# Optimization experiments

Hardware: AMD Instinct MI355X
Metric: run time of the kernel (lower is better)

## Reference

```python
import jax, jax.numpy as jnp
import numpy as np

EPS = 1e-5  # BatchNorm1d default eps
N1, N2 = 4096, 4096


def _encoder(x, W1, b1, W2, b2, W3, b3, gamma, beta):
    # fc1: Linear(node_num,256)+ReLU; fc2: Linear(256,128)+ReLU; fc3: Linear(128,64)+BN(train-mode)+ReLU
    h = jax.nn.relu(x @ W1.T + b1)
    h = jax.nn.relu(h @ W2.T + b2)
    h = h @ W3.T + b3
    m = h.mean(axis=0)
    v = ((h - m) ** 2).mean(axis=0)  # biased variance, as BN training mode
    return jax.nn.relu((h - m) / jnp.sqrt(v + EPS) * gamma + beta)


def _self_attention(x, adj, alpha):
    # vectorized form of the per-node double loop:
    # tmp_i = (sum_{j: adj[i,j]==1} alpha[i,j] * x[j]) / degree_i + x[i]  if degree_i != 0 else 0
    mask = (adj == 1.0).astype(x.dtype)           # [N,N]
    deg = adj.sum(axis=1, keepdims=True)          # [N,1]
    agg = (mask * alpha) @ x                      # [N,64] masked SpMM
    return jnp.where(deg != 0, agg / deg + x, jnp.zeros((), x.dtype))


def setup_inputs() -> dict:
    key = jax.random.key(0)
    ks = jax.random.split(key, 20)
    d = {}
    d["x1"] = jax.random.normal(ks[0], (N1, N1), jnp.float32)
    d["x2"] = jax.random.normal(ks[1], (N2, N2), jnp.float32)
    d["adj1"] = jax.random.bernoulli(ks[2], 0.01, (N1, N1)).astype(jnp.float32)
    d["adj2"] = jax.random.bernoulli(ks[3], 0.01, (N2, N2)).astype(jnp.float32)
    def lin(k, fan_out, fan_in):
        bound = 1.0 / np.sqrt(fan_in)
        k1, k2 = jax.random.split(k)
        return (jax.random.uniform(k1, (fan_out, fan_in), jnp.float32, -bound, bound),
                jax.random.uniform(k2, (fan_out,), jnp.float32, -bound, bound))
    d["e1_W1"], d["e1_b1"] = lin(ks[4], 256, N1)
    d["e1_W2"], d["e1_b2"] = lin(ks[5], 128, 256)
    d["e1_W3"], d["e1_b3"] = lin(ks[6], 64, 128)
    d["e1_gamma"] = jnp.ones((64,), jnp.float32)
    d["e1_beta"] = jnp.zeros((64,), jnp.float32)
    d["e2_W1"], d["e2_b1"] = lin(ks[7], 256, N2)
    d["e2_W2"], d["e2_b2"] = lin(ks[8], 128, 256)
    d["e2_W3"], d["e2_b3"] = lin(ks[9], 64, 128)
    d["e2_gamma"] = jnp.ones((64,), jnp.float32)
    d["e2_beta"] = jnp.zeros((64,), jnp.float32)
    d["alpha1"] = jax.random.uniform(ks[10], (N1, N1), jnp.float32)
    d["alpha2"] = jax.random.uniform(ks[11], (N2, N2), jnp.float32)
    d["Wc"], d["bc"] = lin(ks[12], 2, (N1 + N2) * 64)
    return d


def reference(x1, x2, adj1, adj2,
              e1_W1, e1_b1, e1_W2, e1_b2, e1_W3, e1_b3, e1_gamma, e1_beta,
              e2_W1, e2_b1, e2_W2, e2_b2, e2_W3, e2_b3, e2_gamma, e2_beta,
              alpha1, alpha2, Wc, bc):
    h1 = _encoder(x1, e1_W1, e1_b1, e1_W2, e1_b2, e1_W3, e1_b3, e1_gamma, e1_beta)
    h2 = _encoder(x2, e2_W1, e2_b1, e2_W2, e2_b2, e2_W3, e2_b3, e2_gamma, e2_beta)
    h1 = _self_attention(h1, adj1, alpha1)
    h2 = _self_attention(h2, adj2, alpha2)
    feat = jnp.concatenate([h1, h2], axis=0).reshape(1, -1)  # [1,(N1+N2)*64]
    return feat @ Wc.T + bc  # [1,2] logits (softmax is defined but unused in forward)
```

## Files before the change

kernel.cpp:

```cpp
#include <hip/hip_runtime.h>
#include <cstddef>
#include <cstdint>


#define NN 4096
#define HDIM 64
#define ENC_OUT (NN * HDIM)

typedef _Float16 half8 __attribute__((ext_vector_type(8)));
typedef _Float16 half4 __attribute__((ext_vector_type(4)));
typedef float v4f __attribute__((ext_vector_type(4)));

__device__ __forceinline__ void gld_lds16(const void* g, void* l) {
    __builtin_amdgcn_global_load_lds(
        (const __attribute__((address_space(1))) void*)g,
        (__attribute__((address_space(3))) void*)l, 16, 0, 0);
}

struct GemmP {
    const void*     A[2];
    const _Float16* B[2];
    const float*    bias[2];
    void*           C[2];
};

__global__ __launch_bounds__(1024) void fc1_kernel(GemmP p)
{
    __shared__ char lds[64 * 1024];

    const int tid = threadIdx.x;
    const int wave = tid >> 6, lane = tid & 63;
    const int l16 = lane & 15, quad = lane >> 4;
    const int kg = wave >> 2, ng = wave & 3;
    const int enc = blockIdx.y;
    const int m0 = blockIdx.x * 32;
    const int kOff = kg * 1024;
    constexpr int NS = 16;

    const float* __restrict__ A = (const float*)p.A[enc];
    const _Float16* __restrict__ Bp = p.B[enc];

    const int srow = ng * 8 + (lane >> 3);
    const int sc   = lane & 7;
    const float* asrc = A + (size_t)(m0 + srow) * NN + kOff + sc * 4;

    char* f16kg = &lds[kg * 8192];
    const int wof = srow * 64 + (((sc >> 1) ^ ((srow >> 1) & 3)) * 16) + (sc & 1) * 8;

    const int r0 = l16, r1 = 16 + l16;
    const int rd0 = r0 * 64 + ((quad ^ ((r0 >> 1) & 3)) * 16);
    const int rd1 = r1 * 64 + ((quad ^ ((r1 >> 1) & 3)) * 16);

    const _Float16* bsrc = Bp + (size_t)(ng * 64 + l16) * NN + kOff + quad * 8;

    v4f acc[2][4];
#pragma unroll
    for (int mi = 0; mi < 2; mi++)
#pragma unroll
        for (int ni = 0; ni < 4; ni++) acc[mi][ni] = (v4f){0.f, 0.f, 0.f, 0.f};

    float4 aA[2], aB[2];
    aA[0] = *(const float4*)(asrc);
    aA[1] = *(const float4*)(asrc + 32);

    auto body = [&](int s, float4* cur, float4* nxt, bool last) {
        half8 b[2][4];
#pragma unroll
        for (int kq = 0; kq < 2; kq++)
#pragma unroll
            for (int ni = 0; ni < 4; ni++)
                b[kq][ni] = *(const half8*)(bsrc + (size_t)ni * 16 * NN + s * 64 + kq * 32);
        if (!last) {
            nxt[0] = *(const float4*)(asrc + (s + 1) * 64);
            nxt[1] = *(const float4*)(asrc + (s + 1) * 64 + 32);
        }
        __builtin_amdgcn_sched_barrier(0);

        char* fb = f16kg + (s & 1) * 4096;
#pragma unroll
        for (int j = 0; j < 2; j++) {
            half4 h;
            h[0] = (_Float16)cur[j].x; h[1] = (_Float16)cur[j].y;
            h[2] = (_Float16)cur[j].z; h[3] = (_Float16)cur[j].w;
            *(half4*)(fb + j * 2048 + wof) = h;
        }
        __builtin_amdgcn_s_waitcnt(0xC07F);
        __builtin_amdgcn_sched_barrier(0);
        __builtin_amdgcn_s_barrier();
        __builtin_amdgcn_sched_barrier(0);
        half8 a0k0 = *(const half8*)(fb + rd0);
        half8 a1k0 = *(const half8*)(fb + rd1);
        half8 a0k1 = *(const half8*)(fb + 2048 + rd0);
        half8 a1k1 = *(const half8*)(fb + 2048 + rd1);
#pragma unroll
        for (int ni = 0; ni < 4; ni++) {
            acc[0][ni] = __builtin_amdgcn_mfma_f32_16x16x32_f16(a0k0, b[0][ni], acc[0][ni], 0, 0, 0);
            acc[0][ni] = __builtin_amdgcn_mfma_f32_16x16x32_f16(a0k1, b[1][ni], acc[0][ni], 0, 0, 0);
            acc[1][ni] = __builtin_amdgcn_mfma_f32_16x16x32_f16(a1k0, b[0][ni], acc[1][ni], 0, 0, 0);
            acc[1][ni] = __builtin_amdgcn_mfma_f32_16x16x32_f16(a1k1, b[1][ni], acc[1][ni], 0, 0, 0);
        }
    };

    for (int s = 0; s < NS - 2; s += 2) {
        body(s, aA, aB, false);
        body(s + 1, aB, aA, false);
    }
    body(NS - 2, aA, aB, false);
    body(NS - 1, aB, aA, true);

    __syncthreads();

    if (kg >= 2) {
        const int sidx = (kg - 2) * 4 + ng;
#pragma unroll
        for (int mi = 0; mi < 2; mi++)
#pragma unroll
            for (int ni = 0; ni < 4; ni++)
                *(v4f*)&lds[sidx * 8192 + (mi * 4 + ni) * 1024 + lane * 16] = acc[mi][ni];
    }
    __syncthreads();
    if (kg < 2) {
        const int sidx = kg * 4 + ng;
#pragma unroll
        for (int mi = 0; mi < 2; mi++)
#pragma unroll
            for (int ni = 0; ni < 4; ni++)
                acc[mi][ni] += *(const v4f*)&lds[sidx * 8192 + (mi * 4 + ni) * 1024 + lane * 16];
    }
    __syncthreads();

    if (kg == 1) {
#pragma unroll
        for (int mi = 0; mi < 2; mi++)
#pragma unroll
            for (int ni = 0; ni < 4; ni++)
                *(v4f*)&lds[ng * 8192 + (mi * 4 + ni) * 1024 + lane * 16] = acc[mi][ni];
    }
    __syncthreads();

    if (kg == 0) {
        _Float16* __restrict__ h1 = (_Float16*)p.C[enc];
        const float* __restrict__ bs = p.bias[enc];
#pragma unroll
        for (int mi = 0; mi < 2; mi++)
#pragma unroll
            for (int ni = 0; ni < 4; ni++) {
                v4f v = acc[mi][ni] + *(const v4f*)&lds[ng * 8192 + (mi * 4 + ni) * 1024 + lane * 16];
                const int col = ng * 64 + ni * 16 + l16;
                const float b = bs[col];
#pragma unroll
                for (int i = 0; i < 4; i++) {
                    const int row = m0 + mi * 16 + quad * 4 + i;
                    h1[(size_t)row * 256 + col] = (_Float16)fmaxf(v[i] + b, 0.f);
                }
            }
    }
}

template<int NI, bool A16, int OUT, bool RELU>
__global__ __launch_bounds__(256) void gemm_kernel(GemmP p, int M, int lda, int Ksub)
{
    constexpr int N = NI * 64;
    __shared__ char Bs[NI * 4 * 1024];

    const int tid = threadIdx.x;
    const int wave = tid >> 6, lane = tid & 63;
    const int l16 = lane & 15, quad = lane >> 4;
    const int enc = blockIdx.z, split = blockIdx.x;
    const int m0 = blockIdx.y * 32;
    const int kOff = split * Ksub;
    const int nsteps = Ksub >> 5;

    const _Float16* __restrict__ Bp = p.B[enc];
    const char* Abase = (const char*)p.A[enc];

    const size_t aoff0 = (size_t)(m0 + l16) * lda + kOff + quad * 8;
    const size_t aoff1 = aoff0 + (size_t)16 * lda;

    half8 na0, na1;
    float4 nf0lo, nf0hi, nf1lo, nf1hi;
    auto loadA = [&](int s) {
        if constexpr (A16) {
            const _Float16* A = (const _Float16*)Abase;
            na0 = *(const half8*)(A + aoff0 + s * 32);
            na1 = *(const half8*)(A + aoff1 + s * 32);
        } else {
            const float* A = (const float*)Abase;
            nf0lo = *(const float4*)(A + aoff0 + s * 32);
            nf0hi = *(const float4*)(A + aoff0 + s * 32 + 4);
            nf1lo = *(const float4*)(A + aoff1 + s * 32);
            nf1hi = *(const float4*)(A + aoff1 + s * 32 + 4);
        }
    };

    v4f acc[2][NI];
#pragma unroll
    for (int mi = 0; mi < 2; mi++)
#pragma unroll
        for (int ni = 0; ni < NI; ni++) acc[mi][ni] = (v4f){0.f, 0.f, 0.f, 0.f};

    loadA(0);

    for (int s = 0; s < nsteps; ++s) {
#pragma unroll
        for (int ni = 0; ni < NI; ni++) {
            const int T = wave * NI + ni;
            const _Float16* g = Bp + (size_t)(T * 16 + l16) * lda + kOff + s * 32 + quad * 8;
            gld_lds16(g, &Bs[T * 1024]);
        }
        __builtin_amdgcn_sched_barrier(0);
        half8 ca0, ca1;
        if constexpr (A16) {
            ca0 = na0; ca1 = na1;
        } else {
            ca0[0] = (_Float16)nf0lo.x; ca0[1] = (_Float16)nf0lo.y;
            ca0[2] = (_Float16)nf0lo.z; ca0[3] = (_Float16)nf0lo.w;
            ca0[4] = (_Float16)nf0hi.x; ca0[5] = (_Float16)nf0hi.y;
            ca0[6] = (_Float16)nf0hi.z; ca0[7] = (_Float16)nf0hi.w;
            ca1[0] = (_Float16)nf1lo.x; ca1[1] = (_Float16)nf1lo.y;
            ca1[2] = (_Float16)nf1lo.z; ca1[3] = (_Float16)nf1lo.w;
            ca1[4] = (_Float16)nf1hi.x; ca1[5] = (_Float16)nf1hi.y;
            ca1[6] = (_Float16)nf1hi.z; ca1[7] = (_Float16)nf1hi.w;
        }
        const bool more = (s + 1 < nsteps);
        if (more) loadA(s + 1);
        __builtin_amdgcn_sched_barrier(0);

        if (more) __builtin_amdgcn_s_waitcnt(0x0F72);
        else      __builtin_amdgcn_s_waitcnt(0x0F70);
        __builtin_amdgcn_sched_barrier(0);

#pragma unroll
        for (int ni = 0; ni < NI; ni++) {
            half8 bf = *(const half8*)&Bs[(wave * NI + ni) * 1024 + lane * 16];
            acc[0][ni] = __builtin_amdgcn_mfma_f32_16x16x32_f16(ca0, bf, acc[0][ni], 0, 0, 0);
            acc[1][ni] = __builtin_amdgcn_mfma_f32_16x16x32_f16(ca1, bf, acc[1][ni], 0, 0, 0);
        }
    }

#pragma unroll
    for (int mi = 0; mi < 2; mi++)
#pragma unroll
        for (int ni = 0; ni < NI; ni++) {
            const int col = wave * NI * 16 + ni * 16 + l16;
#pragma unroll
            for (int i = 0; i < 4; i++) {
                const int row = m0 + mi * 16 + quad * 4 + i;
                float v = acc[mi][ni][i];
                v += p.bias[enc][col];
                if (RELU) v = fmaxf(v, 0.f);
                if constexpr (OUT == 0)
                    ((_Float16*)p.C[enc])[(size_t)row * N + col] = (_Float16)v;
                else
                    ((float*)p.C[enc])[(size_t)row * N + col] = v;
            }
        }
}

struct CvtJob { const float* s; _Float16* d; int n4; };
struct CvtP { CvtJob j[6]; };

__global__ __launch_bounds__(256) void cvt_all_kernel(CvtP p)
{
    int i = blockIdx.x * 256 + threadIdx.x;
#pragma unroll
    for (int k = 0; k < 6; k++) {
        if (i < p.j[k].n4) {
            float4 v = ((const float4*)p.j[k].s)[i];
            half4 h;
            h[0] = (_Float16)v.x; h[1] = (_Float16)v.y;
            h[2] = (_Float16)v.z; h[3] = (_Float16)v.w;
            ((half4*)p.j[k].d)[i] = h;
            return;
        }
        i -= p.j[k].n4;
    }
}

__global__ __launch_bounds__(256) void bn_stat1_kernel(const float* __restrict__ h3,
                                                       float* __restrict__ bnp)
{
    const int enc = blockIdx.y, b = blockIdx.x;
    const int c = threadIdx.x & 63, rg = threadIdx.x >> 6;
    const float* h = h3 + (size_t)enc * ENC_OUT + (size_t)b * 128 * HDIM;
    float s = 0.f, q = 0.f;
    for (int r = rg; r < 128; r += 4) {
        float v = h[(size_t)r * HDIM + c];
        s += v; q += v * v;
    }
    __shared__ float ss[4][64], sq[4][64];
    ss[rg][c] = s; sq[rg][c] = q;
    __syncthreads();
    if (threadIdx.x < 64) {
        float S = ss[0][c] + ss[1][c] + ss[2][c] + ss[3][c];
        float Q = sq[0][c] + sq[1][c] + sq[2][c] + sq[3][c];
        bnp[(size_t)(enc * 32 + b) * 128 + c] = S;
        bnp[(size_t)(enc * 32 + b) * 128 + 64 + c] = Q;
    }
}

__global__ void bn_stat2_kernel(const float* __restrict__ bnp, float* __restrict__ stats)
{
    const int enc = blockIdx.x, c = threadIdx.x;
    float s = 0.f, q = 0.f;
    for (int b = 0; b < 32; b++) {
        s += bnp[(size_t)(enc * 32 + b) * 128 + c];
        q += bnp[(size_t)(enc * 32 + b) * 128 + 64 + c];
    }
    float mean = s * (1.f / NN);
    float var = q * (1.f / NN) - mean * mean;
    stats[enc * 128 + c] = mean;
    stats[enc * 128 + 64 + c] = rsqrtf(var + 1e-5f);
}

__global__ __launch_bounds__(256) void bn_apply_kernel(const float* __restrict__ h3,
                                                       const float* __restrict__ stats,
                                                       const float* __restrict__ g0,
                                                       const float* __restrict__ g1,
                                                       const float* __restrict__ be0,
                                                       const float* __restrict__ be1,
                                                       float* __restrict__ hn)
{
    const int idx = blockIdx.x * 256 + threadIdx.x;
    const int enc = idx >> 18;
    const int c = idx & 63;
    const float* g = enc ? g1 : g0;
    const float* be = enc ? be1 : be0;
    const float m = stats[enc * 128 + c];
    const float rs = stats[enc * 128 + 64 + c];
    float v = (h3[idx] - m) * rs * g[c] + be[c];
    hn[idx] = fmaxf(v, 0.f);
}

__global__ __launch_bounds__(256) void att_kernel(const float* __restrict__ adj1,
                                                  const float* __restrict__ adj2,
                                                  const float* __restrict__ al1,
                                                  const float* __restrict__ al2,
                                                  const float* __restrict__ hn,
                                                  float* __restrict__ out)
{
    const int enc = blockIdx.y;
    const float* adj = enc ? adj2 : adj1;
    const float* al = enc ? al2 : al1;
    const float* h = hn + (size_t)enc * ENC_OUT;
    float* o = out + (size_t)enc * ENC_OUT;
    const int i = blockIdx.x;
    const int tid = threadIdx.x;
    const int lane = tid & 63;
    const int w = tid >> 6;

    __shared__ int s_j[192];
    __shared__ float s_w[192];
    __shared__ int s_wc[4];
    __shared__ float s_acc[4][64];

    const float* arow = adj + (size_t)i * NN;

    unsigned long long masks[16];
    int cnt_w = 0;
#pragma unroll
    for (int r = 0; r < 16; ++r) {
        float a = arow[w * 1024 + r * 64 + lane];
        unsigned long long m = __ballot(a == 1.f);
        masks[r] = m;
        cnt_w += __popcll(m);
    }
    if (lane == 0) s_wc[w] = cnt_w;
    __syncthreads();

    const int c0 = s_wc[0], c1 = s_wc[1], c2 = s_wc[2], c3 = s_wc[3];
    const int cnt = c0 + c1 + c2 + c3;
    const int cc = min(cnt, 192);
    int run = (w > 0 ? c0 : 0) + (w > 1 ? c1 : 0) + (w > 2 ? c2 : 0);

#pragma unroll
    for (int r = 0; r < 16; ++r) {
        unsigned long long m = masks[r];
        if ((m >> lane) & 1ull) {
            int pos = run + __popcll(m & ((1ull << lane) - 1ull));
            if (pos < 192) s_j[pos] = w * 1024 + r * 64 + lane;
        }
        run += __popcll(m);
    }
    __syncthreads();

    const float* alrow = al + (size_t)i * NN;
    for (int t = tid; t < cc; t += 256) s_w[t] = alrow[s_j[t]];
    __syncthreads();

    const int c = tid & 63;
    const int g = tid >> 6;
    float acc = 0.f;
    for (int t = g; t < cc; t += 4) acc += s_w[t] * h[(size_t)s_j[t] * HDIM + c];
    s_acc[g][c] = acc;
    __syncthreads();

    if (tid < 64) {
        float r;
        if (cnt != 0) {
            r = (s_acc[0][c] + s_acc[1][c] + s_acc[2][c] + s_acc[3][c]) / (float)cnt
                + h[(size_t)i * HDIM + c];
        } else {
            r = 0.f;
        }
        o[(size_t)i * HDIM + c] = r;
    }
}

#define FDIM (2 * ENC_OUT)

__global__ __launch_bounds__(256) void final_partial_kernel(const float* __restrict__ feat,
                                                            const float* __restrict__ Wc,
                                                            float* __restrict__ partial)
{
    const int gt = blockIdx.x * 256 + threadIdx.x;
    float p0 = 0.f, p1 = 0.f;
    for (int f = gt; f < FDIM; f += 131072) {
        float x = feat[f];
        p0 += x * Wc[f];
        p1 += x * Wc[FDIM + f];
    }
    __shared__ float r0[256], r1[256];
    r0[threadIdx.x] = p0;
    r1[threadIdx.x] = p1;
    __syncthreads();
    for (int off = 128; off > 0; off >>= 1) {
        if (threadIdx.x < off) {
            r0[threadIdx.x] += r0[threadIdx.x + off];
            r1[threadIdx.x] += r1[threadIdx.x + off];
        }
        __syncthreads();
    }
    if (threadIdx.x == 0) {
        partial[blockIdx.x * 2 + 0] = r0[0];
        partial[blockIdx.x * 2 + 1] = r1[0];
    }
}

__global__ __launch_bounds__(256) void final_reduce_kernel(const float* __restrict__ partial,
                                                           const float* __restrict__ bc,
                                                           float* __restrict__ out)
{
    const int t = threadIdx.x;
    float2 v = ((const float2*)partial)[t];
    float2 w = ((const float2*)partial)[t + 256];
    __shared__ float r0[256], r1[256];
    r0[t] = v.x + w.x;
    r1[t] = v.y + w.y;
    __syncthreads();
    for (int off = 128; off > 0; off >>= 1) {
        if (t < off) {
            r0[t] += r0[t + off];
            r1[t] += r1[t + off];
        }
        __syncthreads();
    }
    if (t == 0) {
        out[0] = bc[0] + r0[0];
        out[1] = bc[1] + r1[0];
    }
}


extern "C" void kernel_launch(void* const* d_in, const int* in_sizes, int n_in,
                              void* d_out, int out_size, void* d_ws, size_t ws_size,
                              hipStream_t stream)
{
    const float* x1    = (const float*)d_in[0];
    const float* x2    = (const float*)d_in[1];
    const float* adj1  = (const float*)d_in[2];
    const float* adj2  = (const float*)d_in[3];
    const float* e1_W1 = (const float*)d_in[4];
    const float* e1_b1 = (const float*)d_in[5];
    const float* e1_W2 = (const float*)d_in[6];
    const float* e1_b2 = (const float*)d_in[7];
    const float* e1_W3 = (const float*)d_in[8];
    const float* e1_b3 = (const float*)d_in[9];
    const float* e1_g  = (const float*)d_in[10];
    const float* e1_be = (const float*)d_in[11];
    const float* e2_W1 = (const float*)d_in[12];
    const float* e2_b1 = (const float*)d_in[13];
    const float* e2_W2 = (const float*)d_in[14];
    const float* e2_b2 = (const float*)d_in[15];
    const float* e2_W3 = (const float*)d_in[16];
    const float* e2_b3 = (const float*)d_in[17];
    const float* e2_g  = (const float*)d_in[18];
    const float* e2_be = (const float*)d_in[19];
    const float* alpha1 = (const float*)d_in[20];
    const float* alpha2 = (const float*)d_in[21];
    const float* Wc    = (const float*)d_in[22];
    const float* bc    = (const float*)d_in[23];
    (void)in_sizes; (void)n_in; (void)out_size; (void)ws_size;

    char* w = (char*)d_ws;
    _Float16* W1h = (_Float16*)w;  w += (size_t)2 * 256 * NN * 2;
    _Float16* W2h = (_Float16*)w;  w += (size_t)2 * 128 * 256 * 2;
    _Float16* W3h = (_Float16*)w;  w += (size_t)2 * 64 * 128 * 2;
    _Float16* h1h = (_Float16*)w;  w += (size_t)2 * NN * 256 * 2;
    char* shared8 = w;             w += (size_t)8 * 1024 * 1024;
    float* bnp = (float*)w;        w += (size_t)2 * 32 * 128 * 4;
    float* stats = (float*)w;      w += 256 * 4;
    float* hpart = (float*)w;      w += 1024 * 4;

    _Float16* h2h  = (_Float16*)shared8;
    float* h3  = (float*)(shared8 + 2 * 1024 * 1024);
    float* hn  = (float*)(shared8 + 4 * 1024 * 1024);
    float* att = (float*)(shared8 + 6 * 1024 * 1024);

    const dim3 blk(256);

    CvtP cp;
    cp.j[0] = { e1_W1, W1h,             262144 };
    cp.j[1] = { e2_W1, W1h + 256 * NN,  262144 };
    cp.j[2] = { e1_W2, W2h,             8192 };
    cp.j[3] = { e2_W2, W2h + 128 * 256, 8192 };
    cp.j[4] = { e1_W3, W3h,             2048 };
    cp.j[5] = { e2_W3, W3h + 64 * 128,  2048 };
    cvt_all_kernel<<<dim3(2128), blk, 0, stream>>>(cp);

    GemmP p1 = { {x1, x2}, {W1h, W1h + 256 * NN}, {e1_b1, e2_b1},
                 {h1h, h1h + (size_t)NN * 256} };
    fc1_kernel<<<dim3(NN / 32, 2), dim3(1024), 0, stream>>>(p1);

    GemmP p2 = { {h1h, h1h + (size_t)NN * 256}, {W2h, W2h + 128 * 256}, {e1_b2, e2_b2},
                 {h2h, h2h + (size_t)NN * 128} };
    gemm_kernel<2, true, 0, true><<<dim3(1, NN / 32, 2), blk, 0, stream>>>(p2, NN, 256, 256);

    GemmP p3 = { {h2h, h2h + (size_t)NN * 128}, {W3h, W3h + 64 * 128}, {e1_b3, e2_b3},
                 {h3, h3 + ENC_OUT} };
    gemm_kernel<1, true, 1, false><<<dim3(1, NN / 32, 2), blk, 0, stream>>>(p3, NN, 128, 128);

    bn_stat1_kernel<<<dim3(32, 2), blk, 0, stream>>>(h3, bnp);
    bn_stat2_kernel<<<dim3(2), dim3(64), 0, stream>>>(bnp, stats);
    bn_apply_kernel<<<dim3(2 * ENC_OUT / 256), blk, 0, stream>>>(h3, stats, e1_g, e2_g,
                                                                 e1_be, e2_be, hn);

    att_kernel<<<dim3(NN, 2), blk, 0, stream>>>(adj1, adj2, alpha1, alpha2, hn, att);

    final_partial_kernel<<<dim3(512), blk, 0, stream>>>(att, Wc, hpart);
    final_reduce_kernel<<<dim3(1), blk, 0, stream>>>(hpart, bc, (float*)d_out);
}
```

Baseline: 435.0 us.

## Halve fc1 M-tile to 16 rows with a swizzled 1D grid

The fc1 GEMM now gives each block 16 rows instead of 32 and launches 512 blocks on a 1D grid. The block index is swizzled to decide which encoder and row tile each block takes, and LDS use is halved to 32KB. The aim is more blocks and better spread across the many CUs, which should help hide the fp32 A-load latency. The cost is that each W1 fragment loaded into registers now feeds half as many MFMAs, so B traffic per FLOP doubles.

```diff
diff --git a/kernel.cpp b/kernel.cpp
--- a/kernel.cpp
+++ b/kernel.cpp
@@ -24,80 +24,73 @@
     void*           C[2];
 };
 
-__global__ __launch_bounds__(1024) void fc1_kernel(GemmP p)
-{
-    __shared__ char lds[64 * 1024];
+__global__ __launch_bounds__(1024, 8) void fc1_kernel(GemmP p)
+{
+    __shared__ char lds[32 * 1024];
 
     const int tid = threadIdx.x;
     const int wave = tid >> 6, lane = tid & 63;
     const int l16 = lane & 15, quad = lane >> 4;
     const int kg = wave >> 2, ng = wave & 3;
-    const int enc = blockIdx.y;
-    const int m0 = blockIdx.x * 32;
+
+    const int bid = blockIdx.x;
+    const int swz = (bid & 7) * 64 + (bid >> 3);
+    const int enc = swz >> 8;
+    const int m0  = (swz & 255) * 16;
+
     const int kOff = kg * 1024;
     constexpr int NS = 16;
 
     const float* __restrict__ A = (const float*)p.A[enc];
     const _Float16* __restrict__ Bp = p.B[enc];
 
-    const int srow = ng * 8 + (lane >> 3);
-    const int sc   = lane & 7;
+    const int srow = ng * 4 + (lane >> 4);
+    const int sc   = lane & 15;
     const float* asrc = A + (size_t)(m0 + srow) * NN + kOff + sc * 4;
 
-    char* f16kg = &lds[kg * 8192];
-    const int wof = srow * 64 + (((sc >> 1) ^ ((srow >> 1) & 3)) * 16) + (sc & 1) * 8;
-
-    const int r0 = l16, r1 = 16 + l16;
-    const int rd0 = r0 * 64 + ((quad ^ ((r0 >> 1) & 3)) * 16);
-    const int rd1 = r1 * 64 + ((quad ^ ((r1 >> 1) & 3)) * 16);
+    char* f16kg = &lds[kg * 4096];
+    const int wof = (sc >> 3) * 1024 + srow * 64
+                  + ((((sc & 7) >> 1) ^ ((srow >> 1) & 3)) * 16) + (sc & 1) * 8;
+
+    const int rd0 = l16 * 64 + ((quad ^ ((l16 >> 1) & 3)) * 16);
 
     const _Float16* bsrc = Bp + (size_t)(ng * 64 + l16) * NN + kOff + quad * 8;
 
-    v4f acc[2][4];
-#pragma unroll
-    for (int mi = 0; mi < 2; mi++)
-#pragma unroll
-        for (int ni = 0; ni < 4; ni++) acc[mi][ni] = (v4f){0.f, 0.f, 0.f, 0.f};
-
-    float4 aA[2], aB[2];
-    aA[0] = *(const float4*)(asrc);
-    aA[1] = *(const float4*)(asrc + 32);
-
-    auto body = [&](int s, float4* cur, float4* nxt, bool last) {
+    v4f acc[4];
+#pragma unroll
+    for (int ni = 0; ni < 4; ni++) acc[ni] = (v4f){0.f, 0.f, 0.f, 0.f};
+
+    float4 aA, aB;
+    aA = *(const float4*)(asrc);
+
+    auto body = [&](int s, float4& cur, float4& nxt, bool last) {
         half8 b[2][4];
 #pragma unroll
         for (int kq = 0; kq < 2; kq++)
 #pragma unroll
             for (int ni = 0; ni < 4; ni++)
                 b[kq][ni] = *(const half8*)(bsrc + (size_t)ni * 16 * NN + s * 64 + kq * 32);
-        if (!last) {
-            nxt[0] = *(const float4*)(asrc + (s + 1) * 64);
-            nxt[1] = *(const float4*)(asrc + (s + 1) * 64 + 32);
-        }
+        if (!last)
+            nxt = *(const float4*)(asrc + (s + 1) * 64);
         __builtin_amdgcn_sched_barrier(0);
 
-        char* fb = f16kg + (s & 1) * 4096;
-#pragma unroll
-        for (int j = 0; j < 2; j++) {
+        char* fb = f16kg + (s & 1) * 2048;
+        {
             half4 h;
-            h[0] = (_Float16)cur[j].x; h[1] = (_Float16)cur[j].y;
-            h[2] = (_Float16)cur[j].z; h[3] = (_Float16)cur[j].w;
-            *(half4*)(fb + j * 2048 + wof) = h;
+            h[0] = (_Float16)cur.x; h[1] = (_Float16)cur.y;
+            h[2] = (_Float16)cur.z; h[3] = (_Float16)cur.w;
+            *(half4*)(fb + wof) = h;
         }
         __builtin_amdgcn_s_waitcnt(0xC07F);
         __builtin_amdgcn_sched_barrier(0);
         __builtin_amdgcn_s_barrier();
         __builtin_amdgcn_sched_barrier(0);
-        half8 a0k0 = *(const half8*)(fb + rd0);
-        half8 a1k0 = *(const half8*)(fb + rd1);
-        half8 a0k1 = *(const half8*)(fb + 2048 + rd0);
-        half8 a1k1 = *(const half8*)(fb + 2048 + rd1);
+        half8 ca0 = *(const half8*)(fb + rd0);
+        half8 ca1 = *(const half8*)(fb + 1024 + rd0);
 #pragma unroll
         for (int ni = 0; ni < 4; ni++) {
-            acc[0][ni] = __builtin_amdgcn_mfma_f32_16x16x32_f16(a0k0, b[0][ni], acc[0][ni], 0, 0, 0);
-            acc[0][ni] = __builtin_amdgcn_mfma_f32_16x16x32_f16(a0k1, b[1][ni], acc[0][ni], 0, 0, 0);
-            acc[1][ni] = __builtin_amdgcn_mfma_f32_16x16x32_f16(a1k0, b[0][ni], acc[1][ni], 0, 0, 0);
-            acc[1][ni] = __builtin_amdgcn_mfma_f32_16x16x32_f16(a1k1, b[1][ni], acc[1][ni], 0, 0, 0);
+            acc[ni] = __builtin_amdgcn_mfma_f32_16x16x32_f16(ca0, b[0][ni], acc[ni], 0, 0, 0);
+            acc[ni] = __builtin_amdgcn_mfma_f32_16x16x32_f16(ca1, b[1][ni], acc[ni], 0, 0, 0);
         }
     };
 
@@ -113,28 +106,22 @@
     if (kg >= 2) {
         const int sidx = (kg - 2) * 4 + ng;
 #pragma unroll
-        for (int mi = 0; mi < 2; mi++)
-#pragma unroll
-            for (int ni = 0; ni < 4; ni++)
-                *(v4f*)&lds[sidx * 8192 + (mi * 4 + ni) * 1024 + lane * 16] = acc[mi][ni];
+        for (int ni = 0; ni < 4; ni++)
+            *(v4f*)&lds[sidx * 4096 + ni * 1024 + lane * 16] = acc[ni];
     }
     __syncthreads();
     if (kg < 2) {
         const int sidx = kg * 4 + ng;
 #pragma unroll
-        for (int mi = 0; mi < 2; mi++)
-#pragma unroll
-            for (int ni = 0; ni < 4; ni++)
-                acc[mi][ni] += *(const v4f*)&lds[sidx * 8192 + (mi * 4 + ni) * 1024 + lane * 16];
+        for (int ni = 0; ni < 4; ni++)
+            acc[ni] += *(const v4f*)&lds[sidx * 4096 + ni * 1024 + lane * 16];
     }
     __syncthreads();
 
     if (kg == 1) {
 #pragma unroll
-        for (int mi = 0; mi < 2; mi++)
-#pragma unroll
-            for (int ni = 0; ni < 4; ni++)
-                *(v4f*)&lds[ng * 8192 + (mi * 4 + ni) * 1024 + lane * 16] = acc[mi][ni];
+        for (int ni = 0; ni < 4; ni++)
+            *(v4f*)&lds[ng * 4096 + ni * 1024 + lane * 16] = acc[ni];
     }
     __syncthreads();
 
@@ -142,18 +129,16 @@
         _Float16* __restrict__ h1 = (_Float16*)p.C[enc];
         const float* __restrict__ bs = p.bias[enc];
 #pragma unroll
-        for (int mi = 0; mi < 2; mi++)
-#pragma unroll
-            for (int ni = 0; ni < 4; ni++) {
-                v4f v = acc[mi][ni] + *(const v4f*)&lds[ng * 8192 + (mi * 4 + ni) * 1024 + lane * 16];
-                const int col = ng * 64 + ni * 16 + l16;
-                const float b = bs[col];
-#pragma unroll
-                for (int i = 0; i < 4; i++) {
-                    const int row = m0 + mi * 16 + quad * 4 + i;
-                    h1[(size_t)row * 256 + col] = (_Float16)fmaxf(v[i] + b, 0.f);
-                }
+        for (int ni = 0; ni < 4; ni++) {
+            v4f v = acc[ni] + *(const v4f*)&lds[ng * 4096 + ni * 1024 + lane * 16];
+            const int col = ng * 64 + ni * 16 + l16;
+            const float b = bs[col];
+#pragma unroll
+            for (int i = 0; i < 4; i++) {
+                const int row = m0 + quad * 4 + i;
+                h1[(size_t)row * 256 + col] = (_Float16)fmaxf(v[i] + b, 0.f);
             }
+        }
     }
 }
 
@@ -520,7 +505,7 @@
 
     GemmP p1 = { {x1, x2}, {W1h, W1h + 256 * NN}, {e1_b1, e2_b1},
                  {h1h, h1h + (size_t)NN * 256} };
-    fc1_kernel<<<dim3(NN / 32, 2), dim3(1024), 0, stream>>>(p1);
+    fc1_kernel<<<dim3(512), dim3(1024), 0, stream>>>(p1);
 
     GemmP p2 = { {h1h, h1h + (size_t)NN * 256}, {W2h, W2h + 128 * 256}, {e1_b2, e2_b2},
                  {h2h, h2h + (size_t)NN * 128} };
```

New measurement: 606.8 us. +39.5%, slower.
